# Optimization experiments

Measured on AMD Instinct MI355X. Metric: run time of the kernel, lower is better.

Reference implementation:

```python
import jax, jax.numpy as jnp
import numpy as np

MIN_LEVEL, MAX_LEVEL = 2, 5

# pywt Wavelet('db4') analysis filters (dec_lo / dec_hi)
DEC_LO = np.array([-0.010597401784997278, 0.032883011666982945, 0.030841381835986965,
                   -0.18703481171888114, -0.02798376941698385, 0.6308807679295904,
                   0.7148465705525415, 0.23037781330885523])
DEC_HI = np.array([-0.23037781330885523, 0.7148465705525415, -0.6308807679295904,
                   -0.02798376941698385, 0.18703481171888114, 0.030841381835986965,
                   -0.032883011666982945, -0.010597401784997278])
# pytorch_wavelets time-reverses the filters and uses cross-correlation (F.conv),
# which is exactly what lax.conv_general_dilated computes.
H0 = jnp.asarray(DEC_LO[::-1].copy(), jnp.float32)
H1 = jnp.asarray(DEC_HI[::-1].copy(), jnp.float32)


def _afb1d(x):
    """One-level analysis filter bank, 'zero' padding mode (pytorch_wavelets afb1d).
    x: (N, 1, T) -> (lo, hi) each (N, 1, floor((T+L-1)/2))."""
    T = x.shape[-1]
    L = H0.shape[0]
    out = (T + L - 1) // 2          # pywt.dwt_coeff_len(T, L, 'zero')
    p = 2 * out - T                 # total pad; extra zero goes to the right if odd
    xp = jnp.pad(x, ((0, 0), (0, 0), (p // 2, p - p // 2)))
    k = jnp.stack([H0, H1])[:, None, :]          # (2, 1, L)
    lohi = jax.lax.conv_general_dilated(
        xp, k, window_strides=(2,), padding='VALID',
        dimension_numbers=('NCH', 'OIH', 'NCH'))
    return lohi[:, 0:1, :], lohi[:, 1:2, :]


def _decompose(x, levels):
    """Batched multi-level DWT cascade over all features at once; per-feature
    decomposition level selected afterwards via one-hot / masking (same math as
    the original per-feature Python loop)."""
    B, S, F = x.shape
    cur = jnp.transpose(x, (0, 2, 1)).reshape(B * F, 1, S)
    los, his = [], []
    for _ in range(MAX_LEVEL):
        lo, hi = _afb1d(cur)

        def to_bsf(a):
            # zero-pad coeffs up to seq_len, back to (B, S, F) layout
            a = jnp.pad(a, ((0, 0), (0, 0), (0, S - a.shape[-1])))
            return jnp.transpose(a.reshape(B, F, S), (0, 2, 1))

        los.append(to_bsf(lo))
        his.append(to_bsf(hi))
        cur = lo
    los = jnp.stack(los)   # (MAX_LEVEL, B, S, F) lowpass after level j+1
    his = jnp.stack(his)   # (MAX_LEVEL, B, S, F) detail at level j+1

    # approx for feature f = lowpass after `levels[f]` levels
    sel = jax.nn.one_hot(levels - 1, MAX_LEVEL, dtype=x.dtype)      # (F, MAX_LEVEL)
    approx = jnp.einsum('lbsf,fl->bsf', los, sel)
    # details[i] only populated for i < levels[f]
    mask = (jnp.arange(MAX_LEVEL)[:, None] < levels[None, :]).astype(x.dtype)  # (L, F)
    details = his * mask[:, None, None, :]
    high_freq = details.sum(axis=0)
    low_freq = approx
    return approx, details, high_freq, low_freq


def setup_inputs() -> dict:
    key = jax.random.key(0)
    k1, k2 = jax.random.split(key)
    x = jax.random.normal(k1, (32, 4096, 64), jnp.float32)
    complexity_scores = jax.random.uniform(k2, (64,), jnp.float32)
    return {"x": x, "complexity_scores": complexity_scores}


def reference(x, complexity_scores):
    # level_scaled = min_level + round(score * (max_level - min_level)); Python round
    # and jnp.round both use round-half-to-even.
    levels = MIN_LEVEL + jnp.round(
        complexity_scores * (MAX_LEVEL - MIN_LEVEL)).astype(jnp.int32)
    levels = jnp.clip(levels, MIN_LEVEL, MAX_LEVEL)   # (F,)
    return _decompose(x, levels)
```

## Files before the change

### kernel.cpp

```cpp
#include <hip/hip_runtime.h>


#define NB 32
#define NS 4096
#define NF 64
#define BSF (NB * NS * NF)
#define NF4 (NF / 4)

typedef float f4v __attribute__((ext_vector_type(4)));

__constant__ float c_h0[8] = {
     0.23037781330885523f,  0.7148465705525415f,   0.6308807679295904f,
    -0.02798376941698385f, -0.18703481171888114f,  0.030841381835986965f,
     0.032883011666982945f, -0.010597401784997278f};
__constant__ float c_h1[8] = {
    -0.010597401784997278f, -0.032883011666982945f, 0.030841381835986965f,
     0.18703481171888114f,  -0.02798376941698385f,  -0.6308807679295904f,
     0.7148465705525415f,   -0.23037781330885523f};

__device__ __forceinline__ int get_level(const float* __restrict__ scores, int f) {
    int lv = 2 + (int)rintf(scores[f] * 3.0f);
    return min(5, max(2, lv));
}

template <int J, int TIN, int LOG2LEN>
__global__ __launch_bounds__(256) void wl_lvl(
    const f4v* __restrict__ in, f4v* __restrict__ lo_out,
    f4v* __restrict__ det, const float* __restrict__ scores)
{
    constexpr int LEN = 1 << LOG2LEN;
    int t = blockIdx.x * 256 + threadIdx.x;
    int f4 = t & (NF4 - 1);
    int r = t >> 4;
    int np = r & (LEN / 2 - 1);
    int b = r >> (LOG2LEN - 1);
    int n0 = 2 * np;

    const f4v* row = in + (size_t)b * TIN * NF4 + f4;
    const f4v z = {0.f, 0.f, 0.f, 0.f};
    f4v v[10];
    int base = n0 * 2 - 3;
#pragma unroll
    for (int j = 0; j < 10; ++j) {
        int m = base + j;
        v[j] = ((unsigned)m < (unsigned)TIN) ? row[(size_t)m * NF4] : z;
    }
    f4v lo0 = z, hi0 = z, lo1 = z, hi1 = z;
#pragma unroll
    for (int i = 0; i < 8; ++i) {
        lo0 += c_h0[i] * v[i];      hi0 += c_h1[i] * v[i];
        lo1 += c_h0[i] * v[i + 2];  hi1 += c_h1[i] * v[i + 2];
    }
    if (J >= 3) {
        int f0 = f4 * 4;
#pragma unroll
        for (int c = 0; c < 4; ++c)
            if (get_level(scores, f0 + c) < J) { hi0[c] = 0.f; hi1[c] = 0.f; }
    }
    f4v* lp = lo_out + (size_t)(b * LEN + n0) * NF4 + f4;
    lp[0] = lo0;  lp[NF4] = lo1;
    f4v* dp = det + (size_t)(b * NS + n0) * NF4 + f4;
    dp[0] = hi0;  dp[NF4] = hi1;
}

__global__ __launch_bounds__(256) void wl_final(
    const float* __restrict__ lo2s, const float* __restrict__ lo3s,
    const float* __restrict__ lo4s, f4v* __restrict__ out4,
    const float* __restrict__ scores)
{
    int t = blockIdx.x * 256 + threadIdx.x;
    int f4 = t & (NF4 - 1);
    int r = t >> 4;
    int n = r & (NS - 1);
    int b = r >> 12;
    int f0 = f4 * 4;

    int lv[4];
#pragma unroll
    for (int c = 0; c < 4; ++c) lv[c] = get_level(scores, f0 + c);

    const f4v z = {0.f, 0.f, 0.f, 0.f};
    f4v d5 = z, l5 = z;
    if (n < 128) {
        const f4v* row = (const f4v*)lo4s + (size_t)b * 256 * NF4 + f4;
        int base = 2 * n - 3;
        f4v hi = z;
#pragma unroll
        for (int i = 0; i < 8; ++i) {
            int m = base + i;
            if ((unsigned)m < 256u) {
                f4v v = row[(size_t)m * NF4];
                l5 += c_h0[i] * v;  hi += c_h1[i] * v;
            }
        }
#pragma unroll
        for (int c = 0; c < 4; ++c) d5[c] = (lv[c] >= 5) ? hi[c] : 0.f;
    }

    f4v* det1 = out4 + (size_t)1 * (BSF / 4);
    f4v* det2 = out4 + (size_t)2 * (BSF / 4);
    f4v* det3 = out4 + (size_t)3 * (BSF / 4);
    f4v* det4 = out4 + (size_t)4 * (BSF / 4);

    f4v acc = d5;
    if (n < 2048) {
        acc += det1[t];
        if (n < 1024) acc += det2[t];
        if (n < 512)  acc += det3[t];
        if (n < 256)  acc += det4[t];
    }

    f4v av = z;
#pragma unroll
    for (int c = 0; c < 4; ++c) {
        int L = lv[c];
        int len = 2048 >> (L - 1);
        float vv = 0.f;
        if (n < len) {
            if (L == 5)      vv = l5[c];
            else if (L == 4) vv = lo4s[(size_t)(b * 256 + n) * NF + f0 + c];
            else if (L == 3) vv = lo3s[(size_t)(b * 512 + n) * NF + f0 + c];
            else             vv = lo2s[(size_t)(b * 1024 + n) * NF + f0 + c];
        }
        av[c] = vv;
    }

    __builtin_nontemporal_store(av,  out4 + t);
    __builtin_nontemporal_store(d5,  out4 + (size_t)5 * (BSF / 4) + t);
    __builtin_nontemporal_store(acc, out4 + (size_t)6 * (BSF / 4) + t);
    __builtin_nontemporal_store(av,  out4 + (size_t)7 * (BSF / 4) + t);
    if (n >= 2048) __builtin_nontemporal_store(z, det1 + t);
    if (n >= 1024) __builtin_nontemporal_store(z, det2 + t);
    if (n >= 512)  __builtin_nontemporal_store(z, det3 + t);
    if (n >= 256)  __builtin_nontemporal_store(z, det4 + t);
}

extern "C" void kernel_launch(void* const* d_in, const int* in_sizes, int n_in,
                              void* d_out, int out_size, void* d_ws, size_t ws_size,
                              hipStream_t stream)
{
    const f4v* x        = (const f4v*)d_in[0];
    const float* scores = (const float*)d_in[1];
    f4v* out4 = (f4v*)d_out;
    float* ws = (float*)d_ws;

    f4v* lo1 = (f4v*)ws;
    f4v* lo2 = lo1 + (size_t)NB * 2048 * NF4;
    f4v* lo3 = lo2 + (size_t)NB * 1024 * NF4;
    f4v* lo4 = lo3 + (size_t)NB * 512 * NF4;

    f4v* det1 = out4 + (size_t)1 * (BSF / 4);
    f4v* det2 = out4 + (size_t)2 * (BSF / 4);
    f4v* det3 = out4 + (size_t)3 * (BSF / 4);
    f4v* det4 = out4 + (size_t)4 * (BSF / 4);

    dim3 block(256);
    wl_lvl<1, 4096, 11><<<dim3(NB * 1024 * NF4 / 256), block, 0, stream>>>(x,   lo1, det1, scores);
    wl_lvl<2, 2048, 10><<<dim3(NB *  512 * NF4 / 256), block, 0, stream>>>(lo1, lo2, det2, scores);
    wl_lvl<3, 1024,  9><<<dim3(NB *  256 * NF4 / 256), block, 0, stream>>>(lo2, lo3, det3, scores);
    wl_lvl<4,  512,  8><<<dim3(NB *  128 * NF4 / 256), block, 0, stream>>>(lo3, lo4, det4, scores);
    wl_final<<<dim3(BSF / 4 / 256), block, 0, stream>>>((const float*)lo2, (const float*)lo3,
                                                        (const float*)lo4, out4, scores);
}
```

Measured before the change: 308.1 us.

## Fuse DWT levels 2-5 into one per-batch pyramid kernel with block syncs

Levels 2 through 5 of the cascade now run in a single kernel. Each block owns one batch and a quarter of the features, and __syncthreads separates the levels, replacing three separate launches. Level 1 now makes four outputs per thread from 14 loaded rows instead of two from 10. The final kernel reads a precomputed lo5/det5 instead of recomputing level 5, and loads the scores as one vector. In exchange, the pyramid kernel has only 128 blocks, so parallelism is low, and the loops in the later levels are serial.

```diff
diff --git a/kernel.cpp b/kernel.cpp
--- a/kernel.cpp
+++ b/kernel.cpp
@@ -4,8 +4,8 @@
 #define NB 32
 #define NS 4096
 #define NF 64
+#define NF4 16
 #define BSF (NB * NS * NF)
-#define NF4 (NF / 4)
 
 typedef float f4v __attribute__((ext_vector_type(4)));
 
@@ -18,121 +18,145 @@
      0.18703481171888114f,  -0.02798376941698385f,  -0.6308807679295904f,
      0.7148465705525415f,   -0.23037781330885523f};
 
-__device__ __forceinline__ int get_level(const float* __restrict__ scores, int f) {
-    int lv = 2 + (int)rintf(scores[f] * 3.0f);
-    return min(5, max(2, lv));
+__device__ __forceinline__ void levels4(const float* __restrict__ scores, int f4,
+                                        int lv[4]) {
+    f4v s = ((const f4v*)scores)[f4];
+#pragma unroll
+    for (int c = 0; c < 4; ++c) {
+        int l = 2 + (int)rintf(s[c] * 3.0f);
+        lv[c] = min(5, max(2, l));
+    }
 }
 
-template <int J, int TIN, int LOG2LEN>
-__global__ __launch_bounds__(256) void wl_lvl(
-    const f4v* __restrict__ in, f4v* __restrict__ lo_out,
-    f4v* __restrict__ det, const float* __restrict__ scores)
+__global__ __launch_bounds__(256) void wl_l1(
+    const f4v* __restrict__ x, f4v* __restrict__ lo1, f4v* __restrict__ det1)
 {
-    constexpr int LEN = 1 << LOG2LEN;
     int t = blockIdx.x * 256 + threadIdx.x;
-    int f4 = t & (NF4 - 1);
+    int f4 = t & 15;
     int r = t >> 4;
-    int np = r & (LEN / 2 - 1);
-    int b = r >> (LOG2LEN - 1);
-    int n0 = 2 * np;
+    int nq = r & 511;
+    int b  = r >> 9;
+    int n0 = nq * 4;
 
-    const f4v* row = in + (size_t)b * TIN * NF4 + f4;
     const f4v z = {0.f, 0.f, 0.f, 0.f};
-    f4v v[10];
-    int base = n0 * 2 - 3;
+    const f4v* row = x + (size_t)b * NS * NF4 + f4;
+    f4v v[14];
+    int base = 2 * n0 - 3;
 #pragma unroll
-    for (int j = 0; j < 10; ++j) {
+    for (int j = 0; j < 14; ++j) {
         int m = base + j;
-        v[j] = ((unsigned)m < (unsigned)TIN) ? row[(size_t)m * NF4] : z;
+        v[j] = ((unsigned)m < (unsigned)NS) ? row[(size_t)m * NF4] : z;
     }
-    f4v lo0 = z, hi0 = z, lo1 = z, hi1 = z;
+    f4v* lp = lo1  + (size_t)(b * 2048 + n0) * NF4 + f4;
+    f4v* dp = det1 + (size_t)(b * NS   + n0) * NF4 + f4;
 #pragma unroll
-    for (int i = 0; i < 8; ++i) {
-        lo0 += c_h0[i] * v[i];      hi0 += c_h1[i] * v[i];
-        lo1 += c_h0[i] * v[i + 2];  hi1 += c_h1[i] * v[i + 2];
+    for (int k = 0; k < 4; ++k) {
+        f4v l = z, h = z;
+#pragma unroll
+        for (int i = 0; i < 8; ++i) { l += c_h0[i] * v[2*k + i]; h += c_h1[i] * v[2*k + i]; }
+        lp[k * NF4] = l;
+        dp[k * NF4] = h;
     }
-    if (J >= 3) {
-        int f0 = f4 * 4;
-#pragma unroll
-        for (int c = 0; c < 4; ++c)
-            if (get_level(scores, f0 + c) < J) { hi0[c] = 0.f; hi1[c] = 0.f; }
-    }
-    f4v* lp = lo_out + (size_t)(b * LEN + n0) * NF4 + f4;
-    lp[0] = lo0;  lp[NF4] = lo1;
-    f4v* dp = det + (size_t)(b * NS + n0) * NF4 + f4;
-    dp[0] = hi0;  dp[NF4] = hi1;
 }
 
-__global__ __launch_bounds__(256) void wl_final(
-    const float* __restrict__ lo2s, const float* __restrict__ lo3s,
-    const float* __restrict__ lo4s, f4v* __restrict__ out4,
-    const float* __restrict__ scores)
+template <int TIN, int LEN, int J>
+__device__ __forceinline__ void pyr_level(
+    const f4v* __restrict__ src_base, f4v* __restrict__ lo_out,
+    f4v* __restrict__ det, int b, int f4, int tn, const int lv[4])
+{
+    const f4v z = {0.f, 0.f, 0.f, 0.f};
+    const f4v* src = src_base + (size_t)b * TIN * NF4 + f4;
+#pragma unroll
+    for (int k = 0; k < LEN / 64; ++k) {
+        int n = tn + 64 * k;
+        f4v l = z, h = z;
+        int base = 2 * n - 3;
+#pragma unroll
+        for (int i = 0; i < 8; ++i) {
+            int m = base + i;
+            if ((unsigned)m < (unsigned)TIN) {
+                f4v vv = src[(size_t)m * NF4];
+                l += c_h0[i] * vv;  h += c_h1[i] * vv;
+            }
+        }
+        if (J >= 3) {
+#pragma unroll
+            for (int c = 0; c < 4; ++c) if (lv[c] < J) h[c] = 0.f;
+        }
+        lo_out[(size_t)(b * LEN + n) * NF4 + f4] = l;
+        det[(size_t)(b * NS + n) * NF4 + f4] = h;
+    }
+}
+
+__global__ __launch_bounds__(256) void wl_pyr(
+    const f4v* __restrict__ lo1, f4v* __restrict__ lo2, f4v* __restrict__ lo3,
+    f4v* __restrict__ lo4, f4v* __restrict__ lo5,
+    f4v* __restrict__ det2, f4v* __restrict__ det3, f4v* __restrict__ det4,
+    f4v* __restrict__ det5, const float* __restrict__ scores)
+{
+    int b  = blockIdx.x >> 2;
+    int q  = blockIdx.x & 3;
+    int fl = threadIdx.x & 3;
+    int tn = threadIdx.x >> 2;
+    int f4 = q * 4 + fl;
+    int lv[4];
+    levels4(scores, f4, lv);
+
+    pyr_level<2048, 1024, 2>(lo1, lo2, det2, b, f4, tn, lv);
+    __syncthreads();
+    pyr_level<1024,  512, 3>(lo2, lo3, det3, b, f4, tn, lv);
+    __syncthreads();
+    pyr_level< 512,  256, 4>(lo3, lo4, det4, b, f4, tn, lv);
+    __syncthreads();
+    pyr_level< 256,  128, 5>(lo4, lo5, det5, b, f4, tn, lv);
+}
+
+__global__ __launch_bounds__(256) void wl_out(
+    const f4v* __restrict__ lo2, const f4v* __restrict__ lo3,
+    const f4v* __restrict__ lo4, const f4v* __restrict__ lo5,
+    f4v* __restrict__ out4, const float* __restrict__ scores)
 {
     int t = blockIdx.x * 256 + threadIdx.x;
-    int f4 = t & (NF4 - 1);
+    int f4 = t & 15;
     int r = t >> 4;
     int n = r & (NS - 1);
     int b = r >> 12;
-    int f0 = f4 * 4;
-
     int lv[4];
-#pragma unroll
-    for (int c = 0; c < 4; ++c) lv[c] = get_level(scores, f0 + c);
+    levels4(scores, f4, lv);
 
     const f4v z = {0.f, 0.f, 0.f, 0.f};
-    f4v d5 = z, l5 = z;
-    if (n < 128) {
-        const f4v* row = (const f4v*)lo4s + (size_t)b * 256 * NF4 + f4;
-        int base = 2 * n - 3;
-        f4v hi = z;
-#pragma unroll
-        for (int i = 0; i < 8; ++i) {
-            int m = base + i;
-            if ((unsigned)m < 256u) {
-                f4v v = row[(size_t)m * NF4];
-                l5 += c_h0[i] * v;  hi += c_h1[i] * v;
-            }
-        }
-#pragma unroll
-        for (int c = 0; c < 4; ++c) d5[c] = (lv[c] >= 5) ? hi[c] : 0.f;
-    }
-
     f4v* det1 = out4 + (size_t)1 * (BSF / 4);
     f4v* det2 = out4 + (size_t)2 * (BSF / 4);
     f4v* det3 = out4 + (size_t)3 * (BSF / 4);
     f4v* det4 = out4 + (size_t)4 * (BSF / 4);
+    f4v* det5 = out4 + (size_t)5 * (BSF / 4);
 
-    f4v acc = d5;
-    if (n < 2048) {
-        acc += det1[t];
-        if (n < 1024) acc += det2[t];
-        if (n < 512)  acc += det3[t];
-        if (n < 256)  acc += det4[t];
-    }
+    f4v c2 = (n < 1024) ? lo2[(size_t)(b * 1024 + n) * NF4 + f4] : z;
+    f4v c3 = (n <  512) ? lo3[(size_t)(b *  512 + n) * NF4 + f4] : z;
+    f4v c4 = (n <  256) ? lo4[(size_t)(b *  256 + n) * NF4 + f4] : z;
+    f4v c5 = (n <  128) ? lo5[(size_t)(b *  128 + n) * NF4 + f4] : z;
 
-    f4v av = z;
+    f4v av;
 #pragma unroll
-    for (int c = 0; c < 4; ++c) {
-        int L = lv[c];
-        int len = 2048 >> (L - 1);
-        float vv = 0.f;
-        if (n < len) {
-            if (L == 5)      vv = l5[c];
-            else if (L == 4) vv = lo4s[(size_t)(b * 256 + n) * NF + f0 + c];
-            else if (L == 3) vv = lo3s[(size_t)(b * 512 + n) * NF + f0 + c];
-            else             vv = lo2s[(size_t)(b * 1024 + n) * NF + f0 + c];
-        }
-        av[c] = vv;
-    }
+    for (int c = 0; c < 4; ++c)
+        av[c] = (lv[c] == 2) ? c2[c] : (lv[c] == 3) ? c3[c]
+              : (lv[c] == 4) ? c4[c] : c5[c];
+
+    f4v acc = z;
+    if (n < 2048) acc += det1[t];
+    if (n < 1024) acc += det2[t];
+    if (n <  512) acc += det3[t];
+    if (n <  256) acc += det4[t];
+    if (n <  128) acc += det5[t];
 
     __builtin_nontemporal_store(av,  out4 + t);
-    __builtin_nontemporal_store(d5,  out4 + (size_t)5 * (BSF / 4) + t);
     __builtin_nontemporal_store(acc, out4 + (size_t)6 * (BSF / 4) + t);
     __builtin_nontemporal_store(av,  out4 + (size_t)7 * (BSF / 4) + t);
     if (n >= 2048) __builtin_nontemporal_store(z, det1 + t);
     if (n >= 1024) __builtin_nontemporal_store(z, det2 + t);
-    if (n >= 512)  __builtin_nontemporal_store(z, det3 + t);
-    if (n >= 256)  __builtin_nontemporal_store(z, det4 + t);
+    if (n >=  512) __builtin_nontemporal_store(z, det3 + t);
+    if (n >=  256) __builtin_nontemporal_store(z, det4 + t);
+    if (n >=  128) __builtin_nontemporal_store(z, det5 + t);
 }
 
 extern "C" void kernel_launch(void* const* d_in, const int* in_sizes, int n_in,
@@ -142,23 +166,23 @@
     const f4v* x        = (const f4v*)d_in[0];
     const float* scores = (const float*)d_in[1];
     f4v* out4 = (f4v*)d_out;
-    float* ws = (float*)d_ws;
 
-    f4v* lo1 = (f4v*)ws;
+    f4v* lo1 = (f4v*)d_ws;
     f4v* lo2 = lo1 + (size_t)NB * 2048 * NF4;
     f4v* lo3 = lo2 + (size_t)NB * 1024 * NF4;
-    f4v* lo4 = lo3 + (size_t)NB * 512 * NF4;
+    f4v* lo4 = lo3 + (size_t)NB *  512 * NF4;
+    f4v* lo5 = lo4 + (size_t)NB *  256 * NF4;
 
     f4v* det1 = out4 + (size_t)1 * (BSF / 4);
     f4v* det2 = out4 + (size_t)2 * (BSF / 4);
     f4v* det3 = out4 + (size_t)3 * (BSF / 4);
     f4v* det4 = out4 + (size_t)4 * (BSF / 4);
+    f4v* det5 = out4 + (size_t)5 * (BSF / 4);
 
     dim3 block(256);
-    wl_lvl<1, 4096, 11><<<dim3(NB * 1024 * NF4 / 256), block, 0, stream>>>(x,   lo1, det1, scores);
-    wl_lvl<2, 2048, 10><<<dim3(NB *  512 * NF4 / 256), block, 0, stream>>>(lo1, lo2, det2, scores);
-    wl_lvl<3, 1024,  9><<<dim3(NB *  256 * NF4 / 256), block, 0, stream>>>(lo2, lo3, det3, scores);
-    wl_lvl<4,  512,  8><<<dim3(NB *  128 * NF4 / 256), block, 0, stream>>>(lo3, lo4, det4, scores);
-    wl_final<<<dim3(BSF / 4 / 256), block, 0, stream>>>((const float*)lo2, (const float*)lo3,
-                                                        (const float*)lo4, out4, scores);
+    wl_l1 <<<dim3(NB * 512 * NF4 / 256), block, 0, stream>>>(x, lo1, det1);
+    wl_pyr<<<dim3(NB * 4),              block, 0, stream>>>(lo1, lo2, lo3, lo4, lo5,
+                                                            det2, det3, det4, det5, scores);
+    wl_out<<<dim3(BSF / 4 / 256),       block, 0, stream>>>(lo2, lo3, lo4, lo5,
+                                                            out4, scores);
 }
```

New measurement: 339.1 us. +10.0%, slower.
